# Kernel tuning notes

Measured on AMD Instinct MI355X. Metric: run time of the kernel, lower is better.

## Reference

```python
import jax, jax.numpy as jnp
import numpy as np

N_HEADS = 16
HEAD_DIM = 64
HIDDEN = 1024


def setup_inputs() -> dict:
    key = jax.random.key(0)
    kx, kq, kk, kv, ko = jax.random.split(key, 5)
    B, S = 1, 4096
    # xavier_uniform for Linear(hidden, n_heads*head_dim): limit = sqrt(6/(fan_in+fan_out))
    lim = float(np.sqrt(6.0 / (HIDDEN + N_HEADS * HEAD_DIM)))
    x = jax.random.normal(kx, (B, S, HIDDEN), dtype=jnp.float32)
    wq = jax.random.uniform(kq, (N_HEADS * HEAD_DIM, HIDDEN), jnp.float32, -lim, lim)
    wk = jax.random.uniform(kk, (N_HEADS * HEAD_DIM, HIDDEN), jnp.float32, -lim, lim)
    wv = jax.random.uniform(kv, (N_HEADS * HEAD_DIM, HIDDEN), jnp.float32, -lim, lim)
    wo = jax.random.uniform(ko, (HIDDEN, N_HEADS * HEAD_DIM), jnp.float32, -lim, lim)
    return {"x": x, "wq": wq, "wk": wk, "wv": wv, "wo": wo}


def reference(x, wq, wk, wv, wo):
    B, S, _ = x.shape
    scale = HEAD_DIM ** -0.5
    # project and split heads: [B, H, S, D]
    def proj(w):
        return jnp.einsum('bsh,eh->bse', x, w).reshape(B, S, N_HEADS, HEAD_DIM).transpose(0, 2, 1, 3)
    q, k, v = proj(wq), proj(wk), proj(wv)
    scores = jnp.einsum('bhqd,bhkd->bhqk', q, k) * scale  # [B,H,S,S]
    causal = jnp.tril(jnp.ones((S, S), dtype=bool))
    scores = jnp.where(causal, scores, -jnp.inf)
    probs = jax.nn.softmax(scores, axis=-1)
    out = jnp.einsum('bhqk,bhkd->bhqd', probs, v)  # [B,H,S,D]
    out = out.transpose(0, 2, 1, 3).reshape(B, S, N_HEADS * HEAD_DIM)
    return jnp.einsum('bse,he->bsh', out, wo)
```

## Files before the change

### kernel.cpp

```cpp
#include <hip/hip_runtime.h>
#include <hip/hip_bf16.h>
#include <stdint.h>

typedef unsigned short u16;
typedef float f32x4 __attribute__((ext_vector_type(4)));
typedef __bf16 bf16x8 __attribute__((ext_vector_type(8)));
typedef u16 u16x8 __attribute__((ext_vector_type(8)));

#define GL2LDS16(g, l)                                                          \
  __builtin_amdgcn_global_load_lds(                                             \
      (const __attribute__((address_space(1))) unsigned int*)(g),               \
      (__attribute__((address_space(3))) unsigned int*)(l), 16, 0, 0)

#if __has_builtin(__builtin_amdgcn_exp2f)
#define EXP2(x) __builtin_amdgcn_exp2f(x)
#else
#define EXP2(x) exp2f(x)
#endif

#define SOFTMAX_SC 0.18033688f

__device__ __forceinline__ u16 f2bf(float f) {
  uint32_t u = __builtin_bit_cast(uint32_t, f);
  return (u16)((u + 0x7FFFu + ((u >> 16) & 1u)) >> 16);
}

__device__ __forceinline__ uint32_t cvt_pk_bf16(float lo, float hi) {
  uint32_t r;
  asm("v_cvt_pk_bf16_f32 %0, %1, %2" : "=v"(r) : "v"(lo), "v"(hi));
  return r;
}

__device__ __forceinline__ void cast8(const float* __restrict__ s,
                                      u16* __restrict__ d) {
  const float4* p = (const float4*)s;
  float4 a = p[0], b = p[1];
  uint4 o;
  o.x = cvt_pk_bf16(a.x, a.y);
  o.y = cvt_pk_bf16(a.z, a.w);
  o.z = cvt_pk_bf16(b.x, b.y);
  o.w = cvt_pk_bf16(b.z, b.w);
  *(uint4*)d = o;
}

__global__ __launch_bounds__(256) void cast_kernel(const float* __restrict__ s,
                                                   u16* __restrict__ d, int n) {
  int i = (blockIdx.x * 256 + threadIdx.x) * 8;
  if (i >= n) return;
  cast8(s + i, d + i);
}

__global__ __launch_bounds__(256) void cast4_kernel(const float* __restrict__ s0,
                                                    const float* __restrict__ s1,
                                                    const float* __restrict__ s2,
                                                    const float* __restrict__ s3,
                                                    u16* __restrict__ d) {
  int b = blockIdx.x >> 9;
  int i = ((blockIdx.x & 511) * 256 + threadIdx.x) * 8;
  const float* s = (b == 0) ? s0 : (b == 1) ? s1 : (b == 2) ? s2 : s3;
  cast8(s + i, d + ((size_t)b << 20) + i);
}

__global__ __launch_bounds__(512, 2) void gemm8(const u16* __restrict__ A,
                                                const u16* __restrict__ B,
                                                u16* __restrict__ C, int M,
                                                int N, int K, int scaleq) {
  __shared__ u16 As[2][256 * 64];
  __shared__ u16 Bs[2][256 * 64];
  const int tid = threadIdx.x;
  const int lane = tid & 63;
  const int l15 = lane & 15, lhi = lane >> 4;
  const int wave = tid >> 6;
  const int wm = wave >> 2, wn = wave & 3;
  const int m0 = blockIdx.y * 256, n0 = blockIdx.x * 256;
  const int nt = K >> 6;

  int aoff[2][8], boff[2][4];
#pragma unroll
  for (int ks = 0; ks < 2; ++ks) {
    int sl = ((ks * 4 + lhi) ^ (l15 & 7)) << 4;
#pragma unroll
    for (int m = 0; m < 8; ++m)
      aoff[ks][m] = (wm * 128 + m * 16 + l15) * 128 + sl;
#pragma unroll
    for (int n = 0; n < 4; ++n)
      boff[ks][n] = (wn * 64 + n * 16 + l15) * 128 + sl;
  }

  auto unit = [&](int b, int t, int u) {
    const u16* src = (u < 2) ? A : B;
    const int base = ((u < 2) ? m0 : n0) + (u & 1) * 128;
    u16* lb = ((u < 2) ? As[b] : Bs[b]) + (u & 1) * 128 * 64;
#pragma unroll
    for (int i = 0; i < 2; ++i) {
      int c = tid + i * 512;
      int row = c >> 3, slot = c & 7;
      int scol = (slot ^ (row & 7)) * 8;
      GL2LDS16(src + (size_t)(base + row) * K + t * 64 + scol,
               (char*)lb + c * 16);
    }
  };

  f32x4 acc[8][4] = {};

#pragma unroll
  for (int u = 0; u < 4; ++u) unit(0, 0, u);
  asm volatile("s_waitcnt vmcnt(0)" ::: "memory");
  __builtin_amdgcn_s_barrier();

  int cur = 0;
  for (int t = 0; t < nt; ++t) {
    const bool pre = (t + 1) < nt;
    const char* Ab = (const char*)As[cur];
    const char* Bb = (const char*)Bs[cur];
    bf16x8 af[4], bfr[4];

#pragma unroll
    for (int p = 0; p < 4; ++p) {
      const int ks = p >> 1, mh = p & 1;
#pragma unroll
      for (int j = 0; j < 4; ++j)
        af[j] = *(const bf16x8*)(Ab + aoff[ks][mh * 4 + j]);
      if (mh == 0) {
#pragma unroll
        for (int n = 0; n < 4; ++n)
          bfr[n] = *(const bf16x8*)(Bb + boff[ks][n]);
      }
      if (p < 2 && pre) {
        unit(cur ^ 1, t + 1, p * 2);
        unit(cur ^ 1, t + 1, p * 2 + 1);
      }
      __builtin_amdgcn_s_barrier();
      asm volatile("s_waitcnt lgkmcnt(0)" ::: "memory");
      __builtin_amdgcn_sched_barrier(0);
      __builtin_amdgcn_s_setprio(1);
#pragma unroll
      for (int j = 0; j < 4; ++j)
#pragma unroll
        for (int n = 0; n < 4; ++n)
          acc[mh * 4 + j][n] = __builtin_amdgcn_mfma_f32_16x16x32_bf16(
              af[j], bfr[n], acc[mh * 4 + j][n], 0, 0, 0);
      __builtin_amdgcn_s_setprio(0);
      if (p == 3) asm volatile("s_waitcnt vmcnt(0)" ::: "memory");
      __builtin_amdgcn_s_barrier();
    }
    cur ^= 1;
  }

#pragma unroll
  for (int m = 0; m < 8; ++m) {
    int rbase = m0 + wm * 128 + m * 16 + lhi * 4;
#pragma unroll
    for (int n = 0; n < 4; ++n) {
      int col = n0 + wn * 64 + n * 16 + l15;
      float sc = (scaleq && col < 1024) ? SOFTMAX_SC : 1.0f;
#pragma unroll
      for (int r = 0; r < 4; ++r)
        C[(size_t)(rbase + r) * N + col] = f2bf(acc[m][n][r] * sc);
    }
  }
}

template <typename CT>
__global__ __launch_bounds__(256) void gemm_bt(const u16* __restrict__ A,
                                               const u16* __restrict__ B,
                                               CT* __restrict__ C, int M, int N,
                                               int K) {
  __shared__ u16 As[128 * 32];
  __shared__ u16 Bs[128 * 32];
  const int tid = threadIdx.x;
  const int lane = tid & 63;
  const int l15 = lane & 15, lhi = lane >> 4;
  const int wave = tid >> 6;
  const int wr = (wave >> 1) * 64, wc = (wave & 1) * 64;
  const int m0 = blockIdx.y * 128, n0 = blockIdx.x * 128;

  f32x4 acc[4][4] = {};

  for (int k0 = 0; k0 < K; k0 += 32) {
    __syncthreads();
#pragma unroll
    for (int i = 0; i < 2; ++i) {
      int c = tid + i * 256;
      int row = c >> 2, slot = c & 3;
      int scol = (slot ^ ((row >> 1) & 3)) * 8;
      GL2LDS16(A + (size_t)(m0 + row) * K + k0 + scol, (char*)As + c * 16);
      GL2LDS16(B + (size_t)(n0 + row) * K + k0 + scol, (char*)Bs + c * 16);
    }
    __syncthreads();
    bf16x8 af[4], bfr[4];
#pragma unroll
    for (int mi = 0; mi < 4; ++mi) {
      int row = wr + mi * 16 + l15;
      int byt = row * 64 + ((lhi ^ ((row >> 1) & 3)) << 4);
      af[mi] = *(const bf16x8*)((const char*)As + byt);
    }
#pragma unroll
    for (int ni = 0; ni < 4; ++ni) {
      int row = wc + ni * 16 + l15;
      int byt = row * 64 + ((lhi ^ ((row >> 1) & 3)) << 4);
      bfr[ni] = *(const bf16x8*)((const char*)Bs + byt);
    }
#pragma unroll
    for (int mi = 0; mi < 4; ++mi)
#pragma unroll
      for (int ni = 0; ni < 4; ++ni)
        acc[mi][ni] = __builtin_amdgcn_mfma_f32_16x16x32_bf16(
            af[mi], bfr[ni], acc[mi][ni], 0, 0, 0);
  }

#pragma unroll
  for (int mi = 0; mi < 4; ++mi) {
    int rbase = m0 + wr + mi * 16 + lhi * 4;
#pragma unroll
    for (int ni = 0; ni < 4; ++ni) {
      int col = n0 + wc + ni * 16 + l15;
#pragma unroll
      for (int r = 0; r < 4; ++r) {
        float v = acc[mi][ni][r];
        if constexpr (sizeof(CT) == 2)
          C[(size_t)(rbase + r) * N + col] = (CT)f2bf(v);
        else
          C[(size_t)(rbase + r) * N + col] = v;
      }
    }
  }
}

__global__ __launch_bounds__(256) void vtrans_kernel(const u16* __restrict__ qkv,
                                                     u16* __restrict__ vt) {
  __shared__ u16 t[64][72];
  const int bs = blockIdx.x * 64;
  const int be = blockIdx.y * 64;
  const int tid = threadIdx.x;
#pragma unroll
  for (int i = 0; i < 2; ++i) {
    int c = tid + i * 256, row = c >> 3, col = (c & 7) * 8;
    *(u16x8*)&t[row][col] =
        *(const u16x8*)(qkv + (size_t)(bs + row) * 3072 + 2048 + be + col);
  }
  __syncthreads();
#pragma unroll
  for (int i = 0; i < 2; ++i) {
    int c = tid + i * 256, erow = c >> 3, scol = (c & 7) * 8;
    u16x8 o;
#pragma unroll
    for (int j = 0; j < 8; ++j) o[j] = t[scol + j][erow];
    *(u16x8*)(vt + (size_t)(be + erow) * 4096 + bs + scol) = o;
  }
}

__global__ __launch_bounds__(256) void attn_kernel(const u16* __restrict__ qkv,
                                                   const u16* __restrict__ vt,
                                                   u16* __restrict__ out) {
  const int h = blockIdx.y;
  const int bx = blockIdx.x;
  const int tid = threadIdx.x;
  const int lane = tid & 63, wave = tid >> 6;
  const int l15 = lane & 15, lhi = lane >> 4;

  __shared__ u16 Ks[2][64 * 64];
  __shared__ u16 Vs[2][64 * 64];
  __shared__ u16 Ps[4][16 * 64];
  u16* Pw = Ps[wave];

  int koff[2][4];
#pragma unroll
  for (int ks = 0; ks < 2; ++ks)
#pragma unroll
    for (int nf = 0; nf < 4; ++nf) {
      int row = nf * 16 + l15;
      koff[ks][nf] = row * 128 + ((lhi * 16 + ks * 64) ^ ((row & 7) << 4));
    }
  int poff[4];
#pragma unroll
  for (int nf = 0; nf < 4; ++nf)
    poff[nf] = l15 * 128 + ((nf * 32 + lhi * 8) ^ ((l15 & 7) << 4));

  auto stage = [&](int b, int kb) {
#pragma unroll
    for (int i = 0; i < 2; ++i) {
      int c = tid + i * 256;
      int row = c >> 3, slot = c & 7;
      int scol = (slot ^ (row & 7)) * 8;
      GL2LDS16(qkv + (size_t)(kb * 64 + row) * 3072 + 1024 + h * 64 + scol,
               (char*)(Ks[b]) + c * 16);
      GL2LDS16(vt + (size_t)(h * 64 + row) * 4096 + kb * 64 + scol,
               (char*)(Vs[b]) + c * 16);
    }
  };

  int cur = 0;
  for (int rep = 0; rep < 2; ++rep) {
    const int qb = rep ? (63 - bx) : bx;
    const int q0 = qb * 64 + wave * 16;
    const u16* Qb = qkv + (size_t)(q0 + l15) * 3072 + h * 64;
    bf16x8 qf0 = *(const bf16x8*)(const void*)(Qb + lhi * 8);
    bf16x8 qf1 = *(const bf16x8*)(const void*)(Qb + 32 + lhi * 8);

    f32x4 oa[4] = {};
    float mrow = -1e30f, lrow = 0.f;

    stage(cur, 0);
    asm volatile("s_waitcnt vmcnt(0)" ::: "memory");
    __builtin_amdgcn_s_barrier();

    for (int kb = 0; kb <= qb; ++kb) {
      if (kb < qb) stage(cur ^ 1, kb + 1);

      f32x4 s[4] = {};
#pragma unroll
      for (int ks = 0; ks < 2; ++ks)
#pragma unroll
        for (int nf = 0; nf < 4; ++nf) {
          bf16x8 kf =
              *(const bf16x8*)((const char*)(Ks[cur]) + koff[ks][nf]);
          s[nf] = __builtin_amdgcn_mfma_f32_16x16x32_bf16(kf, ks ? qf1 : qf0,
                                                          s[nf], 0, 0, 0);
        }

      if (kb == qb) {
        const int qloc = wave * 16 + l15;
#pragma unroll
        for (int nf = 0; nf < 4; ++nf)
#pragma unroll
          for (int r = 0; r < 4; ++r)
            if (nf * 16 + lhi * 4 + r > qloc) s[nf][r] = -1e30f;
      }

      float pm0 = fmaxf(fmaxf(s[0][0], s[0][1]), fmaxf(s[0][2], s[0][3]));
      float pm1 = fmaxf(fmaxf(s[1][0], s[1][1]), fmaxf(s[1][2], s[1][3]));
      float pm2 = fmaxf(fmaxf(s[2][0], s[2][1]), fmaxf(s[2][2], s[2][3]));
      float pm3 = fmaxf(fmaxf(s[3][0], s[3][1]), fmaxf(s[3][2], s[3][3]));
      float pm = fmaxf(fmaxf(pm0, pm1), fmaxf(pm2, pm3));
      pm = fmaxf(pm, __shfl_xor(pm, 16));
      pm = fmaxf(pm, __shfl_xor(pm, 32));

      if (__any(pm - mrow > 8.0f)) {
        float mn = fmaxf(mrow, pm);
        float al = EXP2(mrow - mn);
        mrow = mn;
        lrow *= al;
        float alq[4];
#pragma unroll
        for (int r = 0; r < 4; ++r) alq[r] = __shfl(al, lhi * 4 + r, 16);
#pragma unroll
        for (int nf = 0; nf < 4; ++nf)
#pragma unroll
          for (int r = 0; r < 4; ++r) oa[nf][r] *= alq[r];
      }

#pragma unroll
      for (int nf = 0; nf < 4; ++nf)
#pragma unroll
        for (int r = 0; r < 4; ++r) s[nf][r] = EXP2(s[nf][r] - mrow);
      float rs = ((s[0][0] + s[0][1]) + (s[0][2] + s[0][3])) +
                 ((s[1][0] + s[1][1]) + (s[1][2] + s[1][3])) +
                 ((s[2][0] + s[2][1]) + (s[2][2] + s[2][3])) +
                 ((s[3][0] + s[3][1]) + (s[3][2] + s[3][3]));
      rs += __shfl_xor(rs, 16);
      rs += __shfl_xor(rs, 32);
      lrow += rs;

#pragma unroll
      for (int nf = 0; nf < 4; ++nf) {
        uint2 pk;
        pk.x = cvt_pk_bf16(s[nf][0], s[nf][1]);
        pk.y = cvt_pk_bf16(s[nf][2], s[nf][3]);
        *(uint2*)((char*)Pw + poff[nf]) = pk;
      }

      bf16x8 pf[2];
#pragma unroll
      for (int ks = 0; ks < 2; ++ks)
        pf[ks] = *(const bf16x8*)((const char*)Pw + koff[ks][0]);

#pragma unroll
      for (int ks = 0; ks < 2; ++ks)
#pragma unroll
        for (int nf = 0; nf < 4; ++nf) {
          bf16x8 vf =
              *(const bf16x8*)((const char*)(Vs[cur]) + koff[ks][nf]);
          oa[nf] = __builtin_amdgcn_mfma_f32_16x16x32_bf16(pf[ks], vf, oa[nf],
                                                           0, 0, 0);
        }

      asm volatile("s_waitcnt vmcnt(0)" ::: "memory");
      __builtin_amdgcn_s_barrier();
      cur ^= 1;
    }

    float linv[4];
#pragma unroll
    for (int r = 0; r < 4; ++r)
      linv[r] = 1.0f / __shfl(lrow, lhi * 4 + r, 16);
#pragma unroll
    for (int r = 0; r < 4; ++r) {
      int rowg = q0 + lhi * 4 + r;
#pragma unroll
      for (int nf = 0; nf < 4; ++nf)
        out[(size_t)rowg * 1024 + h * 64 + nf * 16 + l15] =
            f2bf(oa[nf][r] * linv[r]);
    }
  }
}

extern "C" void kernel_launch(void* const* d_in, const int* in_sizes, int n_in,
                              void* d_out, int out_size, void* d_ws,
                              size_t ws_size, hipStream_t stream) {
  const float* x = (const float*)d_in[0];
  const float* wq = (const float*)d_in[1];
  const float* wk = (const float*)d_in[2];
  const float* wv = (const float*)d_in[3];
  const float* wo = (const float*)d_in[4];

  u16* xb = (u16*)d_ws;
  u16* wqkv = xb + 4096 * 1024;
  u16* wob = wqkv + 3072 * 1024;
  u16* qkv = wob + 1024 * 1024;
  u16* atn = qkv + (size_t)4096 * 3072;
  u16* vt = xb;

  cast_kernel<<<2048, 256, 0, stream>>>(x, xb, 4096 * 1024);
  cast4_kernel<<<2048, 256, 0, stream>>>(wq, wk, wv, wo, wqkv);

  gemm8<<<dim3(12, 16), 512, 0, stream>>>(xb, wqkv, qkv, 4096, 3072, 1024, 1);
  vtrans_kernel<<<dim3(64, 16), 256, 0, stream>>>(qkv, vt);
  attn_kernel<<<dim3(32, 16), 256, 0, stream>>>(qkv, vt, atn);
  gemm_bt<float><<<dim3(8, 32), 256, 0, stream>>>(atn, wob, (float*)d_out, 4096,
                                                  1024, 1024);
}
```

Baseline: 242.6 us.

## Restructure QKV GEMM pipeline with split half-tiles and XCD swizzle; widen attention blocks

The QKV projection GEMM now stages A and B as separate 128-row halves in four LDS buffers. Global-to-LDS loads for the next K-step are interleaved between MFMA groups using partial vmcnt waits, and block IDs are remapped so adjacent tiles land on the same XCD. The attention kernel moves to 512-thread blocks covering 128 query rows, so each K/V tile staged in LDS is shared by eight waves instead of four. The causal mask is generalised to a per-tile check. These changes add many more barriers and run half as many attention blocks, which could hurt occupancy or latency hiding.

Measured after the change: 238.7 us. About the same (-1.6%).

```diff
diff --git a/kernel.cpp b/kernel.cpp
--- a/kernel.cpp
+++ b/kernel.cpp
@@ -61,90 +61,145 @@
   cast8(s + i, d + ((size_t)b << 20) + i);
 }
 
-__global__ __launch_bounds__(512, 2) void gemm8(const u16* __restrict__ A,
-                                                const u16* __restrict__ B,
-                                                u16* __restrict__ C, int M,
-                                                int N, int K, int scaleq) {
-  __shared__ u16 As[2][256 * 64];
-  __shared__ u16 Bs[2][256 * 64];
+template <int MB>
+__device__ __forceinline__ void mfma16(f32x4 (&acc)[8][4], const bf16x8 (&af)[4],
+                                       const bf16x8 (&bfr)[4]) {
+  asm volatile("s_waitcnt lgkmcnt(0)" ::: "memory");
+  __builtin_amdgcn_sched_barrier(0);
+  __builtin_amdgcn_s_setprio(1);
+#pragma unroll
+  for (int j = 0; j < 4; ++j)
+#pragma unroll
+    for (int n = 0; n < 4; ++n)
+      acc[MB + j][n] = __builtin_amdgcn_mfma_f32_16x16x32_bf16(
+          af[j], bfr[n], acc[MB + j][n], 0, 0, 0);
+  __builtin_amdgcn_s_setprio(0);
+}
+
+__global__ __launch_bounds__(512, 2) void gemm8k(const u16* __restrict__ A,
+                                                 const u16* __restrict__ B,
+                                                 u16* __restrict__ C, int M,
+                                                 int N, int K, int scaleq) {
+  __shared__ u16 As[4][128 * 64];
+  __shared__ u16 Bs[4][128 * 64];
   const int tid = threadIdx.x;
   const int lane = tid & 63;
   const int l15 = lane & 15, lhi = lane >> 4;
   const int wave = tid >> 6;
   const int wm = wave >> 2, wn = wave & 3;
-  const int m0 = blockIdx.y * 256, n0 = blockIdx.x * 256;
+  int bid = blockIdx.y * gridDim.x + blockIdx.x;
+  const int cpx = (gridDim.x * gridDim.y) >> 3;
+  bid = (bid & 7) * cpx + (bid >> 3);
+  const int m0 = (bid / gridDim.x) * 256, n0 = (bid % gridDim.x) * 256;
   const int nt = K >> 6;
 
   int aoff[2][8], boff[2][4];
 #pragma unroll
   for (int ks = 0; ks < 2; ++ks) {
-    int sl = ((ks * 4 + lhi) ^ (l15 & 7)) << 4;
-#pragma unroll
-    for (int m = 0; m < 8; ++m)
-      aoff[ks][m] = (wm * 128 + m * 16 + l15) * 128 + sl;
+    const int sl = ((ks * 4 + lhi) ^ (l15 & 7)) << 4;
+#pragma unroll
+    for (int m = 0; m < 8; ++m) aoff[ks][m] = (m * 16 + l15) * 128 + sl;
 #pragma unroll
     for (int n = 0; n < 4; ++n)
-      boff[ks][n] = (wn * 64 + n * 16 + l15) * 128 + sl;
-  }
-
-  auto unit = [&](int b, int t, int u) {
-    const u16* src = (u < 2) ? A : B;
-    const int base = ((u < 2) ? m0 : n0) + (u & 1) * 128;
-    u16* lb = ((u < 2) ? As[b] : Bs[b]) + (u & 1) * 128 * 64;
+      boff[ks][n] = ((wn & 1) * 64 + n * 16 + l15) * 128 + sl;
+  }
+
+  auto stA = [&](int T, int h) {
+    u16* lb = As[(T & 1) * 2 + h];
 #pragma unroll
     for (int i = 0; i < 2; ++i) {
       int c = tid + i * 512;
-      int row = c >> 3, slot = c & 7;
-      int scol = (slot ^ (row & 7)) * 8;
-      GL2LDS16(src + (size_t)(base + row) * K + t * 64 + scol,
+      int row = c >> 3;
+      int scol = ((c & 7) ^ (row & 7)) * 8;
+      GL2LDS16(A + (size_t)(m0 + h * 128 + row) * K + T * 64 + scol,
                (char*)lb + c * 16);
     }
   };
+  auto stB = [&](int T, int h) {
+    u16* lb = Bs[(T & 1) * 2 + h];
+#pragma unroll
+    for (int i = 0; i < 2; ++i) {
+      int c = tid + i * 512;
+      int row = c >> 3;
+      int scol = ((c & 7) ^ (row & 7)) * 8;
+      GL2LDS16(B + (size_t)(n0 + h * 128 + row) * K + T * 64 + scol,
+               (char*)lb + c * 16);
+    }
+  };
 
   f32x4 acc[8][4] = {};
 
-#pragma unroll
-  for (int u = 0; u < 4; ++u) unit(0, 0, u);
+  stA(0, 0); stA(0, 1); stB(0, 0); stB(0, 1);
   asm volatile("s_waitcnt vmcnt(0)" ::: "memory");
   __builtin_amdgcn_s_barrier();
 
-  int cur = 0;
-  for (int t = 0; t < nt; ++t) {
-    const bool pre = (t + 1) < nt;
-    const char* Ab = (const char*)As[cur];
-    const char* Bb = (const char*)Bs[cur];
+  for (int i = 0; i < nt / 2; ++i) {
+    const int e = 2 * i, o = e + 1;
+    const char* Ae = (const char*)As[wm];
+    const char* Be = (const char*)Bs[wn >> 1];
+    const char* Ao = (const char*)As[2 + wm];
+    const char* Bo = (const char*)Bs[2 + (wn >> 1)];
     bf16x8 af[4], bfr[4];
-
-#pragma unroll
-    for (int p = 0; p < 4; ++p) {
-      const int ks = p >> 1, mh = p & 1;
-#pragma unroll
-      for (int j = 0; j < 4; ++j)
-        af[j] = *(const bf16x8*)(Ab + aoff[ks][mh * 4 + j]);
-      if (mh == 0) {
-#pragma unroll
-        for (int n = 0; n < 4; ++n)
-          bfr[n] = *(const bf16x8*)(Bb + boff[ks][n]);
-      }
-      if (p < 2 && pre) {
-        unit(cur ^ 1, t + 1, p * 2);
-        unit(cur ^ 1, t + 1, p * 2 + 1);
-      }
-      __builtin_amdgcn_s_barrier();
-      asm volatile("s_waitcnt lgkmcnt(0)" ::: "memory");
-      __builtin_amdgcn_sched_barrier(0);
-      __builtin_amdgcn_s_setprio(1);
-#pragma unroll
-      for (int j = 0; j < 4; ++j)
-#pragma unroll
-        for (int n = 0; n < 4; ++n)
-          acc[mh * 4 + j][n] = __builtin_amdgcn_mfma_f32_16x16x32_bf16(
-              af[j], bfr[n], acc[mh * 4 + j][n], 0, 0, 0);
-      __builtin_amdgcn_s_setprio(0);
-      if (p == 3) asm volatile("s_waitcnt vmcnt(0)" ::: "memory");
-      __builtin_amdgcn_s_barrier();
-    }
-    cur ^= 1;
+    const bool pre = (e + 2) < nt;
+
+    stA(o, 0); stA(o, 1);
+    asm volatile("s_waitcnt vmcnt(4)" ::: "memory");
+    __builtin_amdgcn_s_barrier();
+#pragma unroll
+    for (int j = 0; j < 4; ++j) af[j] = *(const bf16x8*)(Ae + aoff[0][j]);
+#pragma unroll
+    for (int n = 0; n < 4; ++n) bfr[n] = *(const bf16x8*)(Be + boff[0][n]);
+    mfma16<0>(acc, af, bfr);
+    __builtin_amdgcn_s_barrier();
+#pragma unroll
+    for (int j = 0; j < 4; ++j) af[j] = *(const bf16x8*)(Ae + aoff[0][4 + j]);
+    stB(o, 0); stB(o, 1);
+    __builtin_amdgcn_s_barrier();
+    mfma16<4>(acc, af, bfr);
+    __builtin_amdgcn_s_barrier();
+#pragma unroll
+    for (int j = 0; j < 4; ++j) af[j] = *(const bf16x8*)(Ae + aoff[1][j]);
+#pragma unroll
+    for (int n = 0; n < 4; ++n) bfr[n] = *(const bf16x8*)(Be + boff[1][n]);
+    __builtin_amdgcn_s_barrier();
+    mfma16<0>(acc, af, bfr);
+    __builtin_amdgcn_s_barrier();
+#pragma unroll
+    for (int j = 0; j < 4; ++j) af[j] = *(const bf16x8*)(Ae + aoff[1][4 + j]);
+    __builtin_amdgcn_s_barrier();
+    mfma16<4>(acc, af, bfr);
+    __builtin_amdgcn_s_barrier();
+    if (pre) {
+      stA(e + 2, 0); stA(e + 2, 1);
+      asm volatile("s_waitcnt vmcnt(4)" ::: "memory");
+    } else {
+      asm volatile("s_waitcnt vmcnt(0)" ::: "memory");
+    }
+    __builtin_amdgcn_s_barrier();
+#pragma unroll
+    for (int j = 0; j < 4; ++j) af[j] = *(const bf16x8*)(Ao + aoff[0][j]);
+#pragma unroll
+    for (int n = 0; n < 4; ++n) bfr[n] = *(const bf16x8*)(Bo + boff[0][n]);
+    mfma16<0>(acc, af, bfr);
+    __builtin_amdgcn_s_barrier();
+#pragma unroll
+    for (int j = 0; j < 4; ++j) af[j] = *(const bf16x8*)(Ao + aoff[0][4 + j]);
+    if (pre) { stB(e + 2, 0); stB(e + 2, 1); }
+    __builtin_amdgcn_s_barrier();
+    mfma16<4>(acc, af, bfr);
+    __builtin_amdgcn_s_barrier();
+#pragma unroll
+    for (int j = 0; j < 4; ++j) af[j] = *(const bf16x8*)(Ao + aoff[1][j]);
+#pragma unroll
+    for (int n = 0; n < 4; ++n) bfr[n] = *(const bf16x8*)(Bo + boff[1][n]);
+    __builtin_amdgcn_s_barrier();
+    mfma16<0>(acc, af, bfr);
+    __builtin_amdgcn_s_barrier();
+#pragma unroll
+    for (int j = 0; j < 4; ++j) af[j] = *(const bf16x8*)(Ao + aoff[1][4 + j]);
+    __builtin_amdgcn_s_barrier();
+    mfma16<4>(acc, af, bfr);
+    __builtin_amdgcn_s_barrier();
   }
 
 #pragma unroll
@@ -250,7 +305,7 @@
   }
 }
 
-__global__ __launch_bounds__(256) void attn_kernel(const u16* __restrict__ qkv,
+__global__ __launch_bounds__(512) void attn_kernel(const u16* __restrict__ qkv,
                                                    const u16* __restrict__ vt,
                                                    u16* __restrict__ out) {
   const int h = blockIdx.y;
@@ -261,7 +316,7 @@
 
   __shared__ u16 Ks[2][64 * 64];
   __shared__ u16 Vs[2][64 * 64];
-  __shared__ u16 Ps[4][16 * 64];
+  __shared__ u16 Ps[8][16 * 64];
   u16* Pw = Ps[wave];
 
   int koff[2][4];
@@ -278,22 +333,20 @@
     poff[nf] = l15 * 128 + ((nf * 32 + lhi * 8) ^ ((l15 & 7) << 4));
 
   auto stage = [&](int b, int kb) {
-#pragma unroll
-    for (int i = 0; i < 2; ++i) {
-      int c = tid + i * 256;
-      int row = c >> 3, slot = c & 7;
-      int scol = (slot ^ (row & 7)) * 8;
-      GL2LDS16(qkv + (size_t)(kb * 64 + row) * 3072 + 1024 + h * 64 + scol,
-               (char*)(Ks[b]) + c * 16);
-      GL2LDS16(vt + (size_t)(h * 64 + row) * 4096 + kb * 64 + scol,
-               (char*)(Vs[b]) + c * 16);
-    }
+    int c = tid;
+    int row = c >> 3, slot = c & 7;
+    int scol = (slot ^ (row & 7)) * 8;
+    GL2LDS16(qkv + (size_t)(kb * 64 + row) * 3072 + 1024 + h * 64 + scol,
+             (char*)(Ks[b]) + c * 16);
+    GL2LDS16(vt + (size_t)(h * 64 + row) * 4096 + kb * 64 + scol,
+             (char*)(Vs[b]) + c * 16);
   };
 
   int cur = 0;
   for (int rep = 0; rep < 2; ++rep) {
-    const int qb = rep ? (63 - bx) : bx;
-    const int q0 = qb * 64 + wave * 16;
+    const int qsb = rep ? (31 - bx) : bx;
+    const int ntile = 2 * qsb + 2;
+    const int q0 = qsb * 128 + wave * 16;
     const u16* Qb = qkv + (size_t)(q0 + l15) * 3072 + h * 64;
     bf16x8 qf0 = *(const bf16x8*)(const void*)(Qb + lhi * 8);
     bf16x8 qf1 = *(const bf16x8*)(const void*)(Qb + 32 + lhi * 8);
@@ -305,8 +358,8 @@
     asm volatile("s_waitcnt vmcnt(0)" ::: "memory");
     __builtin_amdgcn_s_barrier();
 
-    for (int kb = 0; kb <= qb; ++kb) {
-      if (kb < qb) stage(cur ^ 1, kb + 1);
+    for (int kb = 0; kb < ntile; ++kb) {
+      if (kb + 1 < ntile) stage(cur ^ 1, kb + 1);
 
       f32x4 s[4] = {};
 #pragma unroll
@@ -319,13 +372,13 @@
                                                           s[nf], 0, 0, 0);
         }
 
-      if (kb == qb) {
-        const int qloc = wave * 16 + l15;
+      if (kb * 64 + 63 > q0) {
+        const int q = q0 + l15;
 #pragma unroll
         for (int nf = 0; nf < 4; ++nf)
 #pragma unroll
           for (int r = 0; r < 4; ++r)
-            if (nf * 16 + lhi * 4 + r > qloc) s[nf][r] = -1e30f;
+            if (kb * 64 + nf * 16 + lhi * 4 + r > q) s[nf][r] = -1e30f;
       }
 
       float pm0 = fmaxf(fmaxf(s[0][0], s[0][1]), fmaxf(s[0][2], s[0][3]));
@@ -424,9 +477,9 @@
   cast_kernel<<<2048, 256, 0, stream>>>(x, xb, 4096 * 1024);
   cast4_kernel<<<2048, 256, 0, stream>>>(wq, wk, wv, wo, wqkv);
 
-  gemm8<<<dim3(12, 16), 512, 0, stream>>>(xb, wqkv, qkv, 4096, 3072, 1024, 1);
+  gemm8k<<<dim3(12, 16), 512, 0, stream>>>(xb, wqkv, qkv, 4096, 3072, 1024, 1);
   vtrans_kernel<<<dim3(64, 16), 256, 0, stream>>>(qkv, vt);
-  attn_kernel<<<dim3(32, 16), 256, 0, stream>>>(qkv, vt, atn);
+  attn_kernel<<<dim3(16, 16), 512, 0, stream>>>(qkv, vt, atn);
   gemm_bt<float><<<dim3(8, 32), 256, 0, stream>>>(atn, wob, (float*)d_out, 4096,
                                                   1024, 1024);
 }
```
